# Kernel optimization log

Measured on AMD Instinct MI355X. Metric: run time of the kernel, lower is better.

Reference implementation:

```python
import jax, jax.numpy as jnp
import numpy as np

TEXTURE_W, SHAPE_W, INTENSITY_W = 1.0, 0.5, 1.0
EPS = 1e-08


def _conv2d_same(x, k):
    # x: [B,1,H,W], k: [1,1,3,3], zero padding 1 (SAME)
    return jax.lax.conv_general_dilated(
        x, k, window_strides=(1, 1), padding='SAME',
        dimension_numbers=('NCHW', 'OIHW', 'NCHW'))


def _box_mean(x):
    # mean over 3x3 zero-padded window == F.unfold(k=3,pad=1).mean(dim=1) for C=1
    k = jnp.ones((1, 1, 3, 3), x.dtype) / 9.0
    return _conv2d_same(x, k)


def _local_variance(x):
    # mean((patch - patch_mean)^2) == E[x^2] - E[x]^2 over the padded 3x3 window
    m = _box_mean(x)
    m2 = _box_mean(x * x)
    return m2 - m * m


def _intensity_loss(inp, out, mask):
    ms = mask.sum() + EPS
    im = (inp * mask).sum() / ms
    om = (out * mask).sum() / ms
    di, do = inp - im, out - om
    iv = (di * di * mask).sum() / ms
    ov = (do * do * mask).sum() / ms
    isk = (di ** 3 * mask).sum() / (ms * (iv ** 1.5 + EPS))
    osk = (do ** 3 * mask).sum() / (ms * (ov ** 1.5 + EPS))
    iku = (di ** 4 * mask).sum() / (ms * (iv ** 2 + EPS))
    oku = (do ** 4 * mask).sum() / (ms * (ov ** 2 + EPS))
    return (im - om) ** 2 + (iv - ov) ** 2 + (isk - osk) ** 2 + (iku - oku) ** 2


def _texture_loss(inp, out, mask):
    it = _local_variance(inp)
    ot = _local_variance(out)
    return jnp.abs(ot * mask - it * mask).mean()


def _shape_loss(inp, out, mask):
    lap = jnp.array([[0., 1., 0.], [1., -4., 1.], [0., 1., 0.]], inp.dtype).reshape(1, 1, 3, 3)
    il = _conv2d_same(inp, lap)
    ol = _conv2d_same(out, lap)
    return jnp.abs(ol * mask - il * mask).mean()


def setup_inputs() -> dict:
    key = jax.random.key(0)
    k1, k2, k3 = jax.random.split(key, 3)
    shape = (32, 1, 512, 512)
    return {
        'input_img': jax.random.normal(k1, shape, jnp.float32),
        'output_img': jax.random.normal(k2, shape, jnp.float32),
        'roi_mask': jax.random.uniform(k3, shape, jnp.float32),
    }


def reference(input_img, output_img, roi_mask):
    intensity = _intensity_loss(input_img, output_img, roi_mask)
    texture = _texture_loss(input_img, output_img, roi_mask)
    shape = _shape_loss(input_img, output_img, roi_mask)
    total = INTENSITY_W * intensity + TEXTURE_W * texture + SHAPE_W * shape
    # stacked [intensity, texture, shape, total] (dict values in original order)
    return jnp.stack([intensity, texture, shape, total])
```

## Files before the change

kernel.cpp:

```cpp
#include <hip/hip_runtime.h>
#include <math.h>

#define H 512
#define W 512
#define BAND 4
#define NQ 11

__device__ __forceinline__ float2 shfl_up1_f2(float2 v, int lane) {
    float2 r;
    r.x = __shfl_up(v.x, 1);
    r.y = __shfl_up(v.y, 1);
    if (lane == 0) { r.x = 0.0f; r.y = 0.0f; }
    return r;
}
__device__ __forceinline__ float2 shfl_dn1_f2(float2 v, int lane) {
    float2 r;
    r.x = __shfl_down(v.x, 1);
    r.y = __shfl_down(v.y, 1);
    if (lane == 63) { r.x = 0.0f; r.y = 0.0f; }
    return r;
}

__device__ __forceinline__ float2 pk_add(float2 a, float2 b) { return make_float2(a.x + b.x, a.y + b.y); }
__device__ __forceinline__ float2 pk_sub(float2 a, float2 b) { return make_float2(a.x - b.x, a.y - b.y); }
__device__ __forceinline__ float2 pk_mul(float2 a, float2 b) { return make_float2(a.x * b.x, a.y * b.y); }
__device__ __forceinline__ float2 pk_muls(float2 a, float s) { return make_float2(a.x * s, a.y * s); }
__device__ __forceinline__ float2 pk_fma(float2 a, float2 b, float2 c) {
    return make_float2(fmaf(a.x, b.x, c.x), fmaf(a.y, b.y, c.y));
}

__device__ __forceinline__ void load_row_pk(const float* __restrict__ inp,
                                            const float* __restrict__ outp,
                                            size_t off, int y, int x0, float2* dst) {
    if (y < 0 || y >= H) {
        #pragma unroll
        for (int j = 0; j < 8; j++) dst[j] = make_float2(0.0f, 0.0f);
    } else {
        const float4* pi = reinterpret_cast<const float4*>(inp  + off + (size_t)y * W + x0);
        const float4* po = reinterpret_cast<const float4*>(outp + off + (size_t)y * W + x0);
        float4 a = pi[0], b = pi[1];
        float4 c = po[0], d = po[1];
        dst[0] = make_float2(a.x, c.x); dst[1] = make_float2(a.y, c.y);
        dst[2] = make_float2(a.z, c.z); dst[3] = make_float2(a.w, c.w);
        dst[4] = make_float2(b.x, d.x); dst[5] = make_float2(b.y, d.y);
        dst[6] = make_float2(b.z, d.z); dst[7] = make_float2(b.w, d.w);
    }
}

__device__ __forceinline__ void load_mask_row(const float* __restrict__ mask, size_t off,
                                              int y, int x0, float* dst) {
    const float4* p = reinterpret_cast<const float4*>(mask + off + (size_t)y * W + x0);
    float4 a = p[0];
    float4 b = p[1];
    dst[0] = a.x; dst[1] = a.y; dst[2] = a.z; dst[3] = a.w;
    dst[4] = b.x; dst[5] = b.y; dst[6] = b.z; dst[7] = b.w;
}

__global__ __launch_bounds__(256) void radiomics_main(
    const float* __restrict__ inp, const float* __restrict__ outp,
    const float* __restrict__ mask, double* __restrict__ partials)
{
    const int tid = threadIdx.x;
    const int lane = tid & 63;
    const int wib = tid >> 6;
    const int gwave = blockIdx.x * 4 + wib;
    const int b = gwave >> 7;
    const int band = gwave & 127;
    const int y0 = band * BAND;
    const size_t off = (size_t)b * H * W;
    const int x0 = lane * 8;

    float2 P[8], C[8], N[8];
    float  Mk[8];

    load_row_pk(inp, outp, off, y0 - 1, x0, P);
    load_row_pk(inp, outp, off, y0,     x0, C);
    load_row_pk(inp, outp, off, y0 + 1, x0, N);
    load_mask_row(mask, off, y0, x0, Mk);

    float  acc0 = 0.0f, accT = 0.0f, accS = 0.0f;
    float2 am1 = make_float2(0,0), am2 = make_float2(0,0);
    float2 am3 = make_float2(0,0), am4 = make_float2(0,0);

    const float inv9 = 1.0f / 9.0f;

    #pragma unroll
    for (int i = 0; i < BAND; i++) {
        if (i) {
            #pragma unroll
            for (int j = 0; j < 8; j++) { P[j] = C[j]; C[j] = N[j]; }
            load_row_pk(inp, outp, off, y0 + i + 1, x0, N);
            load_mask_row(mask, off, y0 + i, x0, Mk);
        }

        float2 s1[8], s2[8];
        #pragma unroll
        for (int j = 0; j < 8; j++) {
            s1[j] = pk_add(pk_add(P[j], C[j]), N[j]);
            s2[j] = pk_fma(P[j], P[j], pk_fma(C[j], C[j], pk_mul(N[j], N[j])));
        }
        float2 h1l = shfl_up1_f2(s1[7], lane), h1r = shfl_dn1_f2(s1[0], lane);
        float2 h2l = shfl_up1_f2(s2[7], lane), h2r = shfl_dn1_f2(s2[0], lane);
        float2 hcl = shfl_up1_f2(C[7],  lane), hcr = shfl_dn1_f2(C[0],  lane);

        #pragma unroll
        for (int j = 0; j < 8; j++) {
            float2 l1 = (j == 0) ? h1l : s1[j-1];
            float2 r1 = (j == 7) ? h1r : s1[j+1];
            float2 l2 = (j == 0) ? h2l : s2[j-1];
            float2 r2 = (j == 7) ? h2r : s2[j+1];
            float2 mn = pk_muls(pk_add(pk_add(l1, s1[j]), r1), inv9);
            float2 e2 = pk_muls(pk_add(pk_add(l2, s2[j]), r2), inv9);
            float2 tv = pk_fma(make_float2(-mn.x, -mn.y), mn, e2);
            float2 cl = (j == 0) ? hcl : C[j-1];
            float2 cr = (j == 7) ? hcr : C[j+1];
            float2 lp = pk_sub(pk_add(pk_add(pk_sub(s1[j], C[j]), cl), cr),
                               pk_muls(C[j], 4.0f));
            float m = Mk[j];
            accT += fabsf(tv.y * m - tv.x * m);
            accS += fabsf(lp.y * m - lp.x * m);
            acc0 += m;
            float2 X = C[j];
            float2 t = pk_muls(X, m);
            am1 = pk_add(am1, t); t = pk_mul(t, X);
            am2 = pk_add(am2, t); t = pk_mul(t, X);
            am3 = pk_add(am3, t); t = pk_mul(t, X);
            am4 = pk_add(am4, t);
        }
    }

    float acc[NQ] = { acc0, am1.x, am2.x, am3.x, am4.x,
                            am1.y, am2.y, am3.y, am4.y, accT, accS };
    #pragma unroll
    for (int q = 0; q < NQ; q++) {
        float v = acc[q];
        #pragma unroll
        for (int o = 32; o > 0; o >>= 1) v += __shfl_down(v, o);
        acc[q] = v;
    }
    __shared__ double red[4][NQ];
    if (lane == 0) {
        #pragma unroll
        for (int q = 0; q < NQ; q++) red[wib][q] = (double)acc[q];
    }
    __syncthreads();
    if (tid < NQ) {
        double s = red[0][tid] + red[1][tid] + red[2][tid] + red[3][tid];
        partials[(size_t)blockIdx.x * NQ + tid] = s;
    }
}

__global__ __launch_bounds__(256) void radiomics_final(
    const double* __restrict__ partials, int nblk, float* __restrict__ out4, double inv_n)
{
    const int tid = threadIdx.x;
    const int lane = tid & 63;
    const int w = tid >> 6;
    double q[NQ];
    #pragma unroll
    for (int k = 0; k < NQ; k++) q[k] = 0.0;
    for (int i = tid; i < nblk; i += 256) {
        #pragma unroll
        for (int k = 0; k < NQ; k++) q[k] += partials[(size_t)i * NQ + k];
    }
    #pragma unroll
    for (int k = 0; k < NQ; k++) {
        #pragma unroll
        for (int o = 32; o > 0; o >>= 1) q[k] += __shfl_down(q[k], o);
    }
    __shared__ double red[4][NQ];
    if (lane == 0) {
        #pragma unroll
        for (int k = 0; k < NQ; k++) red[w][k] = q[k];
    }
    __syncthreads();
    if (tid == 0) {
        double s[NQ];
        #pragma unroll
        for (int k = 0; k < NQ; k++) s[k] = red[0][k] + red[1][k] + red[2][k] + red[3][k];
        const double EPS = 1e-8;
        double S0 = s[0];
        double ms = S0 + EPS;
        double im = s[1] / ms, om = s[5] / ms;
        double im2 = im * im, im3 = im2 * im, im4 = im2 * im2;
        double om2 = om * om, om3 = om2 * om, om4 = om2 * om2;
        double di2 = s[2] - 2.0*im*s[1] + im2*S0;
        double do2 = s[6] - 2.0*om*s[5] + om2*S0;
        double iv = di2 / ms, ov = do2 / ms;
        double di3 = s[3] - 3.0*im*s[2] + 3.0*im2*s[1] - im3*S0;
        double do3 = s[7] - 3.0*om*s[6] + 3.0*om2*s[5] - om3*S0;
        double isk = di3 / (ms * (iv * sqrt(iv) + EPS));
        double osk = do3 / (ms * (ov * sqrt(ov) + EPS));
        double di4 = s[4] - 4.0*im*s[3] + 6.0*im2*s[2] - 4.0*im3*s[1] + im4*S0;
        double do4 = s[8] - 4.0*om*s[7] + 6.0*om2*s[6] - 4.0*om3*s[5] + om4*S0;
        double iku = di4 / (ms * (iv * iv + EPS));
        double oku = do4 / (ms * (ov * ov + EPS));
        double intensity = (im-om)*(im-om) + (iv-ov)*(iv-ov)
                         + (isk-osk)*(isk-osk) + (iku-oku)*(iku-oku);
        double texture = s[9]  * inv_n;
        double shape   = s[10] * inv_n;
        double total = intensity + texture + 0.5 * shape;
        out4[0] = (float)intensity;
        out4[1] = (float)texture;
        out4[2] = (float)shape;
        out4[3] = (float)total;
    }
}

extern "C" void kernel_launch(void* const* d_in, const int* in_sizes, int n_in,
                              void* d_out, int out_size, void* d_ws, size_t ws_size,
                              hipStream_t stream) {
    const float* inp  = (const float*)d_in[0];
    const float* outp = (const float*)d_in[1];
    const float* mask = (const float*)d_in[2];
    const int total = in_sizes[0];
    const int nimg  = total / (H * W);
    const int nwaves = nimg * (H / BAND);
    const int nblk   = nwaves / 4;
    double* partials = (double*)d_ws;

    radiomics_main<<<nblk, 256, 0, stream>>>(inp, outp, mask, partials);
    const double inv_n = 1.0 / (double)total;
    radiomics_final<<<1, 256, 0, stream>>>(partials, nblk, (float*)d_out, inv_n);
}
```

Measured before the change: 126.5 us.

## Use one-wave blocks and prefetch next row before computing current row

Each block is now a single 64-thread wave that writes its own partial sums directly, which removes the shared-memory reduction and the block barrier. The row loop issues the loads for the next input/output row and mask row before computing the current row, so memory latency can overlap with arithmetic. The cost is more registers for the prefetch buffers, four times more partials for the final kernel to sum, and many small blocks.

```diff
diff --git a/kernel.cpp b/kernel.cpp
--- a/kernel.cpp
+++ b/kernel.cpp
@@ -56,22 +56,20 @@
     dst[4] = b.x; dst[5] = b.y; dst[6] = b.z; dst[7] = b.w;
 }
 
-__global__ __launch_bounds__(256) void radiomics_main(
+__global__ __launch_bounds__(64) void radiomics_main(
     const float* __restrict__ inp, const float* __restrict__ outp,
     const float* __restrict__ mask, double* __restrict__ partials)
 {
-    const int tid = threadIdx.x;
-    const int lane = tid & 63;
-    const int wib = tid >> 6;
-    const int gwave = blockIdx.x * 4 + wib;
+    const int lane = threadIdx.x;
+    const int gwave = blockIdx.x;
     const int b = gwave >> 7;
     const int band = gwave & 127;
     const int y0 = band * BAND;
     const size_t off = (size_t)b * H * W;
     const int x0 = lane * 8;
 
-    float2 P[8], C[8], N[8];
-    float  Mk[8];
+    float2 P[8], C[8], N[8], R[8];
+    float  Mk[8], Mn[8];
 
     load_row_pk(inp, outp, off, y0 - 1, x0, P);
     load_row_pk(inp, outp, off, y0,     x0, C);
@@ -86,11 +84,9 @@
 
     #pragma unroll
     for (int i = 0; i < BAND; i++) {
-        if (i) {
-            #pragma unroll
-            for (int j = 0; j < 8; j++) { P[j] = C[j]; C[j] = N[j]; }
-            load_row_pk(inp, outp, off, y0 + i + 1, x0, N);
-            load_mask_row(mask, off, y0 + i, x0, Mk);
+        if (i < BAND - 1) {
+            load_row_pk(inp, outp, off, y0 + i + 2, x0, R);
+            load_mask_row(mask, off, y0 + i + 1, x0, Mn);
         }
 
         float2 s1[8], s2[8];
@@ -127,6 +123,11 @@
             am3 = pk_add(am3, t); t = pk_mul(t, X);
             am4 = pk_add(am4, t);
         }
+
+        if (i < BAND - 1) {
+            #pragma unroll
+            for (int j = 0; j < 8; j++) { P[j] = C[j]; C[j] = N[j]; N[j] = R[j]; Mk[j] = Mn[j]; }
+        }
     }
 
     float acc[NQ] = { acc0, am1.x, am2.x, am3.x, am4.x,
@@ -138,15 +139,10 @@
         for (int o = 32; o > 0; o >>= 1) v += __shfl_down(v, o);
         acc[q] = v;
     }
-    __shared__ double red[4][NQ];
     if (lane == 0) {
         #pragma unroll
-        for (int q = 0; q < NQ; q++) red[wib][q] = (double)acc[q];
-    }
-    __syncthreads();
-    if (tid < NQ) {
-        double s = red[0][tid] + red[1][tid] + red[2][tid] + red[3][tid];
-        partials[(size_t)blockIdx.x * NQ + tid] = s;
+        for (int q = 0; q < NQ; q++)
+            partials[(size_t)gwave * NQ + q] = (double)acc[q];
     }
 }
 
@@ -216,10 +212,9 @@
     const int total = in_sizes[0];
     const int nimg  = total / (H * W);
     const int nwaves = nimg * (H / BAND);
-    const int nblk   = nwaves / 4;
     double* partials = (double*)d_ws;
 
-    radiomics_main<<<nblk, 256, 0, stream>>>(inp, outp, mask, partials);
+    radiomics_main<<<nwaves, 64, 0, stream>>>(inp, outp, mask, partials);
     const double inv_n = 1.0 / (double)total;
-    radiomics_final<<<1, 256, 0, stream>>>(partials, nblk, (float*)d_out, inv_n);
-}
+    radiomics_final<<<1, 256, 0, stream>>>(partials, nwaves, (float*)d_out, inv_n);
+}
```

New measurement: 132.0 us. 4.4% more time.
